# Optimization experiments

Hardware: AMD Instinct MI355X
Metric: run time of the kernel (lower is better)

The kernel has to match this reference:

```python
import jax, jax.numpy as jnp
import numpy as np

B, C, H, W = 2, 3, 96, 96
OC = 2  # conv output channels
EPS = 1e-5

def setup_inputs() -> dict:
    key = jax.random.key(0)
    k1, k2, k3, k4 = jax.random.split(key, 4)
    return {
        "X_tnext": jax.random.normal(k1, (B, C, H, W), dtype=jnp.float32),
        "X_hat_tnext": jax.random.normal(k2, (B, C, H, W), dtype=jnp.float32),
        "conv_w": jax.random.normal(k3, (OC, C, 3, 3), dtype=jnp.float32) * 0.1,
        "conv_b": jax.random.normal(k4, (OC,), dtype=jnp.float32) * 0.1,
        "gamma": jnp.ones((OC,), dtype=jnp.float32),
        "beta": jnp.zeros((OC,), dtype=jnp.float32),
    }

def reference(X_tnext, X_hat_tnext, conv_w, conv_b, gamma, beta):
    b, c, h, w = X_tnext.shape
    n = h * w
    q = X_tnext.reshape(b, c, n)
    k = X_hat_tnext.reshape(b, c, n)
    # corr4D: [b, n, n] = q^T k / sqrt(c)  (materialized O(N^2) volume, as in source)
    corr = jnp.einsum('bcn,bcm->bnm', q, k) / jnp.sqrt(jnp.asarray(c, jnp.float32))
    # weighted aggregation: corr @ X_tnext (broadcast over channels)
    agg = jnp.einsum('bnm,bcm->bcn', corr, q).reshape(b, c, h, w)
    # Conv2d(3->2, k=3, s=1, p=1)
    y = jax.lax.conv_general_dilated(
        agg, conv_w, window_strides=(1, 1), padding='SAME',
        dimension_numbers=('NCHW', 'OIHW', 'NCHW'))
    y = y + conv_b[None, :, None, None]
    # BatchNorm2d (training-mode batch statistics, biased var, eps=1e-5)
    mean = jnp.mean(y, axis=(0, 2, 3), keepdims=True)
    var = jnp.var(y, axis=(0, 2, 3), keepdims=True)
    y = (y - mean) * jax.lax.rsqrt(var + EPS)
    y = y * gamma[None, :, None, None] + beta[None, :, None, None]
    # LeakyReLU(0.1)
    return jnp.where(y >= 0, y, 0.1 * y)
```

## Files before the change

kernel.cpp:

```cpp
#include <hip/hip_runtime.h>
#include <math.h>

namespace {
constexpr int kB = 2, kC = 3, kOC = 2, kH = 96, kW = 96;
constexpr int kN      = kH * kW;
constexpr int kChunks = kN / 256;
constexpr float kEps   = 1e-5f;
constexpr float kScale = 0.57735026918962576f;
constexpr int WS_M = 0;
constexpr int WS_P = 32;
constexpr int WS_Y = 512;
}

__global__ __launch_bounds__(256) void k1_gram(const float* __restrict__ X,
                                               const float* __restrict__ Xh,
                                               float* __restrict__ ws) {
    const int idx = blockIdx.x;
    const int b = idx / 9, cp = (idx % 9) / 3, c = idx % 3;
    const float4* kp = (const float4*)(Xh + (size_t)(b * kC + cp) * kN);
    const float4* qp = (const float4*)(X  + (size_t)(b * kC + c ) * kN);
    float part = 0.f;
    for (int n = threadIdx.x; n < kN / 4; n += 256) {
        const float4 a = kp[n], q = qp[n];
        part += a.x * q.x + a.y * q.y + a.z * q.z + a.w * q.w;
    }
    #pragma unroll
    for (int off = 32; off > 0; off >>= 1) part += __shfl_down(part, off);
    __shared__ float sw[4];
    if ((threadIdx.x & 63) == 0) sw[threadIdx.x >> 6] = part;
    __syncthreads();
    if (threadIdx.x == 0) ws[WS_M + idx] = sw[0] + sw[1] + sw[2] + sw[3];
}

__global__ __launch_bounds__(256) void k2_conv(const float* __restrict__ X,
                                               const float* __restrict__ cw,
                                               const float* __restrict__ cb,
                                               float* __restrict__ ws) {
    const int tid = threadIdx.x;
    const int blk = blockIdx.x;
    const int b   = blk / kChunks;
    const int pix = (blk % kChunks) * 256 + tid;
    const int h = pix / kW, w = pix % kW;

    __shared__ float sM[9];
    __shared__ float sE[2][3][9];
    if (tid < 9) sM[tid] = ws[WS_M + b * 9 + tid];
    __syncthreads();
    if (tid < 54) {
        const int oc = tid / 27, r = tid % 27, cp = r / 9, nb = r % 9;
        sE[oc][cp][nb] = kScale * (cw[oc * 27 +      nb] * sM[cp * 3 + 0] +
                                   cw[oc * 27 +  9 + nb] * sM[cp * 3 + 1] +
                                   cw[oc * 27 + 18 + nb] * sM[cp * 3 + 2]);
    }
    __syncthreads();

    const float* qb = X + (size_t)b * kC * kN;
    float acc0 = cb[0], acc1 = cb[1];
    #pragma unroll
    for (int dh = 0; dh < 3; ++dh) {
        const int hh = h + dh - 1;
        if (hh < 0 || hh >= kH) continue;
        #pragma unroll
        for (int dw = 0; dw < 3; ++dw) {
            const int ww = w + dw - 1;
            if (ww < 0 || ww >= kW) continue;
            const int p = hh * kW + ww, nb = dh * 3 + dw;
            const float q0 = qb[p], q1 = qb[kN + p], q2 = qb[2 * kN + p];
            acc0 += q0 * sE[0][0][nb] + q1 * sE[0][1][nb] + q2 * sE[0][2][nb];
            acc1 += q0 * sE[1][0][nb] + q1 * sE[1][1][nb] + q2 * sE[1][2][nb];
        }
    }
    ws[WS_Y + (b * kOC + 0) * kN + pix] = acc0;
    ws[WS_Y + (b * kOC + 1) * kN + pix] = acc1;

    float v0 = acc0, v1 = acc0 * acc0, v2 = acc1, v3 = acc1 * acc1;
    #pragma unroll
    for (int off = 32; off > 0; off >>= 1) {
        v0 += __shfl_down(v0, off); v1 += __shfl_down(v1, off);
        v2 += __shfl_down(v2, off); v3 += __shfl_down(v3, off);
    }
    __shared__ float sP[4][4];
    if ((tid & 63) == 0) {
        const int wv = tid >> 6;
        sP[wv][0] = v0; sP[wv][1] = v1; sP[wv][2] = v2; sP[wv][3] = v3;
    }
    __syncthreads();
    if (tid < 4) ws[WS_P + blk * 4 + tid] = sP[0][tid] + sP[1][tid] + sP[2][tid] + sP[3][tid];
}

__global__ __launch_bounds__(256) void k3_bn(const float* __restrict__ ws,
                                             const float* __restrict__ gamma,
                                             const float* __restrict__ beta,
                                             float* __restrict__ out) {
    const int tid = threadIdx.x;
    const int i   = blockIdx.x * 256 + tid;
    const int oc  = (i / kN) & 1;
    __shared__ float sS[128], sQ[128];
    if (tid < 128) {
        float s = 0.f, q = 0.f;
        if (tid < 72) {
            s = ws[WS_P + tid * 4 + oc * 2];
            q = ws[WS_P + tid * 4 + oc * 2 + 1];
        }
        sS[tid] = s; sQ[tid] = q;
    }
    __syncthreads();
    for (int st = 64; st > 0; st >>= 1) {
        if (tid < st) { sS[tid] += sS[tid + st]; sQ[tid] += sQ[tid + st]; }
        __syncthreads();
    }
    const float inv  = 1.f / (float)(kB * kN);
    const float mean = sS[0] * inv;
    const float var  = sQ[0] * inv - mean * mean;
    const float g    = gamma[oc] * rsqrtf(var + kEps);
    const float bt   = beta[oc];
    const float y = (ws[WS_Y + i] - mean) * g + bt;
    out[i] = (y >= 0.f) ? y : 0.1f * y;
}

extern "C" void kernel_launch(void* const* d_in, const int* in_sizes, int n_in,
                              void* d_out, int out_size, void* d_ws, size_t ws_size,
                              hipStream_t stream) {
    const float* X      = (const float*)d_in[0];
    const float* Xhat   = (const float*)d_in[1];
    const float* conv_w = (const float*)d_in[2];
    const float* conv_b = (const float*)d_in[3];
    const float* gamma  = (const float*)d_in[4];
    const float* beta   = (const float*)d_in[5];
    float* ws  = (float*)d_ws;

    k1_gram<<<kB * 9, 256, 0, stream>>>(X, Xhat, ws);
    k2_conv<<<kB * kChunks, 256, 0, stream>>>(X, conv_w, conv_b, ws);
    k3_bn  <<<kB * kOC * kChunks, 256, 0, stream>>>(ws, gamma, beta, (float*)d_out);
}
```

Baseline: 73.60 us.

## Fuse Gram computation into conv kernel and interleave conv output as float2

Removes the separate Gram-matrix kernel. Each conv block now redundantly computes the full 3x3 Gram matrix for its batch by reading all of X and Xhat for that batch, which saves one kernel launch. The conv output is stored interleaved as float2 per pixel, so the BN kernel uses half as many blocks, each handling both output channels and reducing all four statistics at once. The cost is redundant global reads: each of 72 blocks reads about 221KB, which L2 mostly serves.

Measured after the change: 71.85 us. 2.4% less time.

```diff
diff --git a/kernel.cpp b/kernel.cpp
--- a/kernel.cpp
+++ b/kernel.cpp
@@ -5,34 +5,15 @@
 constexpr int kB = 2, kC = 3, kOC = 2, kH = 96, kW = 96;
 constexpr int kN      = kH * kW;
 constexpr int kChunks = kN / 256;
+constexpr int kBlocks = kB * kChunks;
 constexpr float kEps   = 1e-5f;
 constexpr float kScale = 0.57735026918962576f;
-constexpr int WS_M = 0;
-constexpr int WS_P = 32;
+constexpr int WS_P = 0;
 constexpr int WS_Y = 512;
 }
 
-__global__ __launch_bounds__(256) void k1_gram(const float* __restrict__ X,
+__global__ __launch_bounds__(256) void kA_conv(const float* __restrict__ X,
                                                const float* __restrict__ Xh,
-                                               float* __restrict__ ws) {
-    const int idx = blockIdx.x;
-    const int b = idx / 9, cp = (idx % 9) / 3, c = idx % 3;
-    const float4* kp = (const float4*)(Xh + (size_t)(b * kC + cp) * kN);
-    const float4* qp = (const float4*)(X  + (size_t)(b * kC + c ) * kN);
-    float part = 0.f;
-    for (int n = threadIdx.x; n < kN / 4; n += 256) {
-        const float4 a = kp[n], q = qp[n];
-        part += a.x * q.x + a.y * q.y + a.z * q.z + a.w * q.w;
-    }
-    #pragma unroll
-    for (int off = 32; off > 0; off >>= 1) part += __shfl_down(part, off);
-    __shared__ float sw[4];
-    if ((threadIdx.x & 63) == 0) sw[threadIdx.x >> 6] = part;
-    __syncthreads();
-    if (threadIdx.x == 0) ws[WS_M + idx] = sw[0] + sw[1] + sw[2] + sw[3];
-}
-
-__global__ __launch_bounds__(256) void k2_conv(const float* __restrict__ X,
                                                const float* __restrict__ cw,
                                                const float* __restrict__ cb,
                                                float* __restrict__ ws) {
@@ -42,9 +23,37 @@
     const int pix = (blk % kChunks) * 256 + tid;
     const int h = pix / kW, w = pix % kW;
 
+    const float*  qb  = X  + (size_t)b * kC * kN;
+    const float4* qb4 = (const float4*)qb;
+    const float4* kb4 = (const float4*)(Xh + (size_t)b * kC * kN);
+    float m[9] = {0,0,0,0,0,0,0,0,0};
+    for (int n = tid; n < kN / 4; n += 256) {
+        const float4 q0 = qb4[n], q1 = qb4[kN/4 + n], q2 = qb4[2*kN/4 + n];
+        const float4 k0 = kb4[n], k1 = kb4[kN/4 + n], k2 = kb4[2*kN/4 + n];
+        m[0] += k0.x*q0.x + k0.y*q0.y + k0.z*q0.z + k0.w*q0.w;
+        m[1] += k0.x*q1.x + k0.y*q1.y + k0.z*q1.z + k0.w*q1.w;
+        m[2] += k0.x*q2.x + k0.y*q2.y + k0.z*q2.z + k0.w*q2.w;
+        m[3] += k1.x*q0.x + k1.y*q0.y + k1.z*q0.z + k1.w*q0.w;
+        m[4] += k1.x*q1.x + k1.y*q1.y + k1.z*q1.z + k1.w*q1.w;
+        m[5] += k1.x*q2.x + k1.y*q2.y + k1.z*q2.z + k1.w*q2.w;
+        m[6] += k2.x*q0.x + k2.y*q0.y + k2.z*q0.z + k2.w*q0.w;
+        m[7] += k2.x*q1.x + k2.y*q1.y + k2.z*q1.z + k2.w*q1.w;
+        m[8] += k2.x*q2.x + k2.y*q2.y + k2.z*q2.z + k2.w*q2.w;
+    }
+    #pragma unroll
+    for (int off = 32; off > 0; off >>= 1) {
+        #pragma unroll
+        for (int j = 0; j < 9; ++j) m[j] += __shfl_down(m[j], off);
+    }
+    __shared__ float sMw[4][9];
     __shared__ float sM[9];
     __shared__ float sE[2][3][9];
-    if (tid < 9) sM[tid] = ws[WS_M + b * 9 + tid];
+    if ((tid & 63) == 0) {
+        #pragma unroll
+        for (int j = 0; j < 9; ++j) sMw[tid >> 6][j] = m[j];
+    }
+    __syncthreads();
+    if (tid < 9) sM[tid] = sMw[0][tid] + sMw[1][tid] + sMw[2][tid] + sMw[3][tid];
     __syncthreads();
     if (tid < 54) {
         const int oc = tid / 27, r = tid % 27, cp = r / 9, nb = r % 9;
@@ -54,7 +63,6 @@
     }
     __syncthreads();
 
-    const float* qb = X + (size_t)b * kC * kN;
     float acc0 = cb[0], acc1 = cb[1];
     #pragma unroll
     for (int dh = 0; dh < 3; ++dh) {
@@ -70,8 +78,7 @@
             acc1 += q0 * sE[1][0][nb] + q1 * sE[1][1][nb] + q2 * sE[1][2][nb];
         }
     }
-    ws[WS_Y + (b * kOC + 0) * kN + pix] = acc0;
-    ws[WS_Y + (b * kOC + 1) * kN + pix] = acc1;
+    ((float2*)(ws + WS_Y))[(size_t)b * kN + pix] = make_float2(acc0, acc1);
 
     float v0 = acc0, v1 = acc0 * acc0, v2 = acc1, v3 = acc1 * acc1;
     #pragma unroll
@@ -85,37 +92,45 @@
         sP[wv][0] = v0; sP[wv][1] = v1; sP[wv][2] = v2; sP[wv][3] = v3;
     }
     __syncthreads();
-    if (tid < 4) ws[WS_P + blk * 4 + tid] = sP[0][tid] + sP[1][tid] + sP[2][tid] + sP[3][tid];
+    if (tid < 4)
+        ws[WS_P + blk * 4 + tid] = sP[0][tid] + sP[1][tid] + sP[2][tid] + sP[3][tid];
 }
 
-__global__ __launch_bounds__(256) void k3_bn(const float* __restrict__ ws,
+__global__ __launch_bounds__(256) void kB_bn(const float* __restrict__ ws,
                                              const float* __restrict__ gamma,
                                              const float* __restrict__ beta,
                                              float* __restrict__ out) {
     const int tid = threadIdx.x;
-    const int i   = blockIdx.x * 256 + tid;
-    const int oc  = (i / kN) & 1;
-    __shared__ float sS[128], sQ[128];
+    const int blk = blockIdx.x;
+    const int b   = blk / kChunks;
+    const int pix = (blk % kChunks) * 256 + tid;
+
+    __shared__ float4 sR[128];
     if (tid < 128) {
-        float s = 0.f, q = 0.f;
-        if (tid < 72) {
-            s = ws[WS_P + tid * 4 + oc * 2];
-            q = ws[WS_P + tid * 4 + oc * 2 + 1];
-        }
-        sS[tid] = s; sQ[tid] = q;
+        float4 p = make_float4(0.f, 0.f, 0.f, 0.f);
+        if (tid < kBlocks) p = ((const float4*)(ws + WS_P))[tid];
+        sR[tid] = p;
     }
     __syncthreads();
-    for (int st = 64; st > 0; st >>= 1) {
-        if (tid < st) { sS[tid] += sS[tid + st]; sQ[tid] += sQ[tid + st]; }
+    for (int s = 64; s > 0; s >>= 1) {
+        if (tid < s) {
+            float4 a = sR[tid], c = sR[tid + s];
+            sR[tid] = make_float4(a.x + c.x, a.y + c.y, a.z + c.z, a.w + c.w);
+        }
         __syncthreads();
     }
-    const float inv  = 1.f / (float)(kB * kN);
-    const float mean = sS[0] * inv;
-    const float var  = sQ[0] * inv - mean * mean;
-    const float g    = gamma[oc] * rsqrtf(var + kEps);
-    const float bt   = beta[oc];
-    const float y = (ws[WS_Y + i] - mean) * g + bt;
-    out[i] = (y >= 0.f) ? y : 0.1f * y;
+    const float4 tot = sR[0];
+    const float inv   = 1.f / (float)(kB * kN);
+    const float mean0 = tot.x * inv, mean1 = tot.z * inv;
+    const float g0 = gamma[0] * rsqrtf(tot.y * inv - mean0 * mean0 + kEps);
+    const float g1 = gamma[1] * rsqrtf(tot.w * inv - mean1 * mean1 + kEps);
+    const float b0 = beta[0], b1 = beta[1];
+
+    const float2 y2 = ((const float2*)(ws + WS_Y))[(size_t)b * kN + pix];
+    float y0 = (y2.x - mean0) * g0 + b0;
+    float y1 = (y2.y - mean1) * g1 + b1;
+    out[(size_t)(b * kOC + 0) * kN + pix] = (y0 >= 0.f) ? y0 : 0.1f * y0;
+    out[(size_t)(b * kOC + 1) * kN + pix] = (y1 >= 0.f) ? y1 : 0.1f * y1;
 }
 
 extern "C" void kernel_launch(void* const* d_in, const int* in_sizes, int n_in,
@@ -127,9 +142,8 @@
     const float* conv_b = (const float*)d_in[3];
     const float* gamma  = (const float*)d_in[4];
     const float* beta   = (const float*)d_in[5];
-    float* ws  = (float*)d_ws;
+    float* ws = (float*)d_ws;
 
-    k1_gram<<<kB * 9, 256, 0, stream>>>(X, Xhat, ws);
-    k2_conv<<<kB * kChunks, 256, 0, stream>>>(X, conv_w, conv_b, ws);
-    k3_bn  <<<kB * kOC * kChunks, 256, 0, stream>>>(ws, gamma, beta, (float*)d_out);
+    kA_conv<<<kBlocks, 256, 0, stream>>>(X, Xhat, conv_w, conv_b, ws);
+    kB_bn  <<<kBlocks, 256, 0, stream>>>(ws, gamma, beta, (float*)d_out);
 }
```
